# Performance work log

Measured on AMD Instinct MI355X. Metric: run time of the kernel, lower is better.

The kernel has to match this reference:

```python
import jax, jax.numpy as jnp
import numpy as np

DAMPENING = 50.0
THR = 1.0
TAU = 10.0
DECAY = float(np.exp(-1.0 / TAU))
V_MIN = -1.0


@jax.custom_vjp
def spike_fn(v_scaled):
    # Heaviside spike with surrogate (triangular) gradient
    return (v_scaled > 0.0).astype(v_scaled.dtype)

def _spike_fwd(v_scaled):
    return spike_fn(v_scaled), v_scaled

def _spike_bwd(v_scaled, dy):
    return (dy * DAMPENING * jnp.maximum(0.0, 1.0 - jnp.abs(v_scaled)),)

spike_fn.defvjp(_spike_fwd, _spike_bwd)


def setup_inputs() -> dict:
    key = jax.random.key(0)
    T, B, N_IN, N = 256, 32, 256, 2048
    ks = jax.random.split(key, 4)
    x = jax.random.normal(ks[0], (T, B, N_IN), jnp.float32)
    W_in = jax.random.normal(ks[1], (N_IN, N), jnp.float32) * (1.0 / np.sqrt(N_IN))
    b = jnp.zeros((N,), jnp.float32)
    # original uses stddev 1/sqrt(n_in) for Bernoulli_weights as well
    W_bern = jax.random.normal(ks[2], (N, N), jnp.float32) * (1.0 / np.sqrt(N_IN))
    random_indices = jax.random.randint(ks[3], (T, N), 0, N)
    return {"x": x, "W_in": W_in, "b": b, "W_bern": W_bern,
            "random_indices": random_indices}


def reference(x, W_in, b, W_bern, random_indices):
    # x: [T, B, n_in]; states v, z2: [B, n]
    B, N = x.shape[1], W_in.shape[1]
    v0 = jnp.zeros((B, N), x.dtype)
    z2_0 = jnp.zeros((B, N), x.dtype)  # old_spike state (unused in math, as in original)

    def step(carry, inp):
        v, _old_z2 = carry
        xt, idx = inp
        i_in = xt @ W_in + b                               # [B, n]
        new_v = jnp.clip(DECAY * v + i_in, V_MIN, THR + 0.01)
        z = spike_fn(new_v - THR)                          # spikes [B, n]
        new_v = jnp.where(z > 0.0, V_MIN, new_v)           # hard reset
        z2 = jnp.take(z @ W_bern, idx, axis=1)             # stochastic projection + column gather
        return (new_v, z2), (z, new_v, z2)

    _, (zs, vs, z2s) = jax.lax.scan(step, (v0, z2_0), (x, random_indices))
    return jnp.stack([zs, vs, z2s], axis=0)  # [3, T, B, n]
```

## Files before the change

### kernel.cpp

```cpp
#include <hip/hip_runtime.h>
#include <hip/hip_bf16.h>
#include <stdint.h>


#define T_STEPS 256
#define BATCH   32
#define NIN     256
#define NN      2048
#define BN_FLAT (BATCH * NN)
#define TBN     (T_STEPS * BATCH * NN)
#define MROWS   (T_STEPS * BATCH)

typedef __attribute__((ext_vector_type(4))) float fx4;
typedef __attribute__((ext_vector_type(4))) int   ix4;

__device__ __forceinline__ void gll16(const void* g, void* l) {
  typedef __attribute__((address_space(1))) void gvoid_t;
  typedef __attribute__((address_space(3))) void lvoid_t;
  __builtin_amdgcn_global_load_lds((gvoid_t*)(g), (lvoid_t*)(l), 16, 0, 0);
}

__device__ __forceinline__ void mfma16(fx4& d, ix4 a, ix4 b) {
  asm volatile("v_mfma_f32_16x16x32_bf16 %0, %1, %2, %0" : "+v"(d) : "v"(a), "v"(b));
}

__global__ __launch_bounds__(256) void xt_k(const float* __restrict__ X,
                                            float* __restrict__ Xt) {
  __shared__ float tile[32][33];
  const int m0 = blockIdx.x << 5, k0 = blockIdx.y << 5;
  const int tx = threadIdx.x, ty = threadIdx.y;
#pragma unroll
  for (int i = 0; i < 32; i += 8)
    tile[ty + i][tx] = X[(size_t)(m0 + ty + i) * NIN + k0 + tx];
  __syncthreads();
#pragma unroll
  for (int i = 0; i < 32; i += 8)
    Xt[(size_t)(k0 + ty + i) * MROWS + m0 + tx] = tile[tx][ty + i];
}

__global__ __launch_bounds__(256) void wt_convert(const float* __restrict__ W,
                                                  __hip_bfloat16* __restrict__ Wt) {
  __shared__ float tile[32][33];
  const int k0 = blockIdx.y << 5, n0 = blockIdx.x << 5;
  const int tx = threadIdx.x, ty = threadIdx.y;
#pragma unroll
  for (int i = 0; i < 32; i += 8)
    tile[ty + i][tx] = W[(size_t)(k0 + ty + i) * NN + n0 + tx];
  __syncthreads();
#pragma unroll
  for (int i = 0; i < 32; i += 8)
    Wt[(size_t)(n0 + ty + i) * NN + k0 + tx] = __float2bfloat16(tile[tx][ty + i]);
}

__global__ __launch_bounds__(256) void in_gemm(const float* __restrict__ Xt,
                                               const float* __restrict__ Wi,
                                               const float* __restrict__ bias,
                                               float* __restrict__ I) {
  __shared__ __align__(16) float As[16 * 64];
  __shared__ __align__(16) float Bs[16 * 128];
  const int tid = threadIdx.x;
  const int tm = tid >> 4;
  const int tn = tid & 15;
  const int m0 = blockIdx.x * 64, n0 = blockIdx.y * 128;

  fx4 acc[4][2] = {};

  const float* gA = Xt + (size_t)(tid >> 4) * MROWS + m0 + (tid & 15) * 4;
  const float* gB = Wi + (size_t)(tid >> 5) * NN + n0 + (tid & 31) * 4;
  char* lA = (char*)As + tid * 16;
  char* lB = (char*)Bs + tid * 16;

  for (int k0 = 0; k0 < NIN; k0 += 16) {
    gll16(gA, lA);
    gll16(gB, lB);
    gll16(gB + 8 * NN, lB + 4096);
    gA += (size_t)16 * MROWS;
    gB += (size_t)16 * NN;
    __syncthreads();
#pragma unroll
    for (int kk = 0; kk < 16; ++kk) {
      fx4 a  = *(const fx4*)&As[kk * 64 + tm * 4];
      fx4 b0 = *(const fx4*)&Bs[kk * 128 + tn * 4];
      fx4 b1 = *(const fx4*)&Bs[kk * 128 + 64 + tn * 4];
#pragma unroll
      for (int r = 0; r < 4; ++r)
#pragma unroll
        for (int c = 0; c < 4; ++c) {
          acc[r][0][c] = fmaf(a[r], b0[c], acc[r][0][c]);
          acc[r][1][c] = fmaf(a[r], b1[c], acc[r][1][c]);
        }
    }
    __syncthreads();
  }

#pragma unroll
  for (int r = 0; r < 4; ++r) {
    const size_t row = (size_t)(m0 + tm * 4 + r) * NN;
    fx4 r0, r1;
#pragma unroll
    for (int c = 0; c < 4; ++c) {
      r0[c] = acc[r][0][c] + bias[n0 + tn * 4 + c];
      r1[c] = acc[r][1][c] + bias[n0 + 64 + tn * 4 + c];
    }
    *(fx4*)&I[row + n0 + tn * 4] = r0;
    *(fx4*)&I[row + n0 + 64 + tn * 4] = r1;
  }
}

__device__ __forceinline__ void scan_body(float* zs, float* vsout,
                                          const float* I, __hip_bfloat16* Zb) {
  const int nid = blockIdx.x * 256 + threadIdx.x;
  float v = 0.f;
  for (int t0 = 0; t0 < T_STEPS; t0 += 8) {
    float iin[8];
#pragma unroll
    for (int u = 0; u < 8; ++u)
      iin[u] = I[(size_t)(t0 + u) * BN_FLAT + nid];
#pragma unroll
    for (int u = 0; u < 8; ++u) {
      float nv = __fadd_rn(__fmul_rn(0.9048374180359595f, v), iin[u]);
      nv = fminf(fmaxf(nv, -1.0f), 1.01f);
      const bool sp = nv > 1.0f;
      const float z = sp ? 1.0f : 0.0f;
      nv = sp ? -1.0f : nv;
      const size_t off = (size_t)(t0 + u) * BN_FLAT + nid;
      zs[off] = z;
      vsout[off] = nv;
      Zb[off] = __float2bfloat16(z);
      v = nv;
    }
  }
}

__global__ __launch_bounds__(256) void scan_sep(float* __restrict__ out,
                                                const float* __restrict__ I,
                                                __hip_bfloat16* __restrict__ Zb) {
  scan_body(out, out + (size_t)TBN, I, Zb);
}

__global__ __launch_bounds__(256) void scan_inp(float* out, __hip_bfloat16* Zb) {
  scan_body(out, out + (size_t)TBN, out + (size_t)TBN, Zb);
}

__global__ __launch_bounds__(256) void bern_gemm(const __hip_bfloat16* __restrict__ Z,
                                                 const __hip_bfloat16* __restrict__ Wt,
                                                 float* __restrict__ Y) {
  __shared__ __align__(16) __hip_bfloat16 Asm[128 * 32];
  __shared__ __align__(16) __hip_bfloat16 Bsm[128 * 32];
  const int tid = threadIdx.x;
  const int lane = tid & 63;
  const int wid = tid >> 6;
  const int wr = wid >> 1, wc = wid & 1;
  const int m0 = blockIdx.x * 128, n0 = blockIdx.y * 128;

  fx4 acc[4][4] = {};

  const int trow = tid >> 2;
  const int tcol = (tid & 3) << 4;
  const char* gA = (const char*)Z + ((size_t)(m0 + trow) << 12) + tcol;
  const char* gB = (const char*)Wt + ((size_t)(n0 + trow) << 12) + tcol;
  char* lA = (char*)Asm + tid * 16;
  char* lB = (char*)Bsm + tid * 16;

  const ix4* Au = (const ix4*)Asm;
  const ix4* Bu = (const ix4*)Bsm;
  const int abase = (wr * 64 + (lane & 15)) * 4 + (lane >> 4);
  const int bbase = (wc * 64 + (lane & 15)) * 4 + (lane >> 4);

  for (int ks = 0; ks < 64; ++ks) {
    gll16(gA, lA);
    gll16(gA + (size_t)64 * 4096, lA + 4096);
    gll16(gB, lB);
    gll16(gB + (size_t)64 * 4096, lB + 4096);
    gA += 64;
    gB += 64;
    __syncthreads();

    ix4 af[4], bf[4];
#pragma unroll
    for (int i = 0; i < 4; ++i) af[i] = Au[abase + i * 64];
#pragma unroll
    for (int i = 0; i < 4; ++i) bf[i] = Bu[bbase + i * 64];
#pragma unroll
    for (int mf = 0; mf < 4; ++mf)
#pragma unroll
      for (int nf = 0; nf < 4; ++nf)
        mfma16(acc[mf][nf], af[mf], bf[nf]);
    __syncthreads();
  }

  asm volatile("s_nop 7\n\ts_nop 7");

  const int crow = (lane >> 4) * 4;
  const int ccol = lane & 15;
#pragma unroll
  for (int mf = 0; mf < 4; ++mf)
#pragma unroll
    for (int nf = 0; nf < 4; ++nf)
#pragma unroll
      for (int j = 0; j < 4; ++j) {
        const int r = m0 + wr * 64 + mf * 16 + crow + j;
        const int c = n0 + wc * 64 + nf * 16 + ccol;
        Y[(size_t)r * NN + c] = acc[mf][nf][j];
      }
}

__global__ __launch_bounds__(256) void gather_k(float* __restrict__ Y,
                                                const int* __restrict__ ridx) {
  __shared__ __align__(16) float rowbuf[NN];
  const int tb = blockIdx.x;
  const int t = tb >> 5;
  float* yrow = Y + (size_t)tb * NN;
  const int tid = threadIdx.x;
#pragma unroll
  for (int i = 0; i < 2; ++i) {
    int u = tid + i * 256;
    ((fx4*)rowbuf)[u] = ((const fx4*)yrow)[u];
  }
  __syncthreads();
  const int* ir = ridx + t * NN;
#pragma unroll
  for (int i = 0; i < 8; ++i) {
    int j = tid + i * 256;
    yrow[j] = rowbuf[ir[j]];
  }
}

extern "C" void kernel_launch(void* const* d_in, const int* in_sizes, int n_in,
                              void* d_out, int out_size, void* d_ws, size_t ws_size,
                              hipStream_t stream) {
  const float* x      = (const float*)d_in[0];
  const float* W_in   = (const float*)d_in[1];
  const float* bias   = (const float*)d_in[2];
  const float* W_bern = (const float*)d_in[3];
  const int*   ridx   = (const int*)d_in[4];
  float* out = (float*)d_out;
  char* ws = (char*)d_ws;

  __hip_bfloat16* Wt = (__hip_bfloat16*)ws;
  __hip_bfloat16* Zb = (__hip_bfloat16*)(ws + (size_t)8388608);
  const size_t offI = 41943040;
  const bool sep = ws_size >= (size_t)109051904;
  float* Ibuf = sep ? (float*)(ws + offI) : (out + (size_t)TBN);

  float* Xt = out;

  xt_k<<<dim3(256, 8), dim3(32, 8), 0, stream>>>(x, Xt);
  wt_convert<<<dim3(64, 64), dim3(32, 8), 0, stream>>>(W_bern, Wt);
  in_gemm<<<dim3(128, 16), dim3(256), 0, stream>>>(Xt, W_in, bias, Ibuf);
  if (sep)
    scan_sep<<<dim3(256), dim3(256), 0, stream>>>(out, Ibuf, Zb);
  else
    scan_inp<<<dim3(256), dim3(256), 0, stream>>>(out, Zb);
  bern_gemm<<<dim3(64, 16), dim3(256), 0, stream>>>(Zb, Wt, out + (size_t)2 * TBN);
  gather_k<<<dim3(8192), dim3(256), 0, stream>>>(out + (size_t)2 * TBN, ridx);
}
```

Measured before the change: 253.0 us.

## Rewrite Bernoulli GEMM with 256x256 tiles, double-buffered LDS, and swizzled loads

```diff
diff --git a/kernel.cpp b/kernel.cpp
--- a/kernel.cpp
+++ b/kernel.cpp
@@ -142,66 +142,109 @@
   scan_body(out, out + (size_t)TBN, out + (size_t)TBN, Zb);
 }
 
-__global__ __launch_bounds__(256) void bern_gemm(const __hip_bfloat16* __restrict__ Z,
-                                                 const __hip_bfloat16* __restrict__ Wt,
-                                                 float* __restrict__ Y) {
-  __shared__ __align__(16) __hip_bfloat16 Asm[128 * 32];
-  __shared__ __align__(16) __hip_bfloat16 Bsm[128 * 32];
+__global__ __launch_bounds__(512, 2) void bern_gemm(const __hip_bfloat16* __restrict__ Z,
+                                                    const __hip_bfloat16* __restrict__ Wt,
+                                                    float* __restrict__ Y) {
+  __shared__ __align__(16) char lds[131072];
   const int tid = threadIdx.x;
-  const int lane = tid & 63;
-  const int wid = tid >> 6;
-  const int wr = wid >> 1, wc = wid & 1;
-  const int m0 = blockIdx.x * 128, n0 = blockIdx.y * 128;
-
-  fx4 acc[4][4] = {};
-
-  const int trow = tid >> 2;
-  const int tcol = (tid & 3) << 4;
-  const char* gA = (const char*)Z + ((size_t)(m0 + trow) << 12) + tcol;
-  const char* gB = (const char*)Wt + ((size_t)(n0 + trow) << 12) + tcol;
-  char* lA = (char*)Asm + tid * 16;
-  char* lB = (char*)Bsm + tid * 16;
-
-  const ix4* Au = (const ix4*)Asm;
-  const ix4* Bu = (const ix4*)Bsm;
-  const int abase = (wr * 64 + (lane & 15)) * 4 + (lane >> 4);
-  const int bbase = (wc * 64 + (lane & 15)) * 4 + (lane >> 4);
-
-  for (int ks = 0; ks < 64; ++ks) {
-    gll16(gA, lA);
-    gll16(gA + (size_t)64 * 4096, lA + 4096);
-    gll16(gB, lB);
-    gll16(gB + (size_t)64 * 4096, lB + 4096);
-    gA += 64;
-    gB += 64;
-    __syncthreads();
-
-    ix4 af[4], bf[4];
-#pragma unroll
-    for (int i = 0; i < 4; ++i) af[i] = Au[abase + i * 64];
-#pragma unroll
-    for (int i = 0; i < 4; ++i) bf[i] = Bu[bbase + i * 64];
-#pragma unroll
-    for (int mf = 0; mf < 4; ++mf)
-#pragma unroll
-      for (int nf = 0; nf < 4; ++nf)
-        mfma16(acc[mf][nf], af[mf], bf[nf]);
-    __syncthreads();
-  }
-
-  asm volatile("s_nop 7\n\ts_nop 7");
-
-  const int crow = (lane >> 4) * 4;
-  const int ccol = lane & 15;
-#pragma unroll
-  for (int mf = 0; mf < 4; ++mf)
-#pragma unroll
-    for (int nf = 0; nf < 4; ++nf)
+  const int l = tid & 63, wid = tid >> 6;
+  const int wr = wid >> 2, wc = wid & 3;
+  const int l15 = l & 15, l4 = l >> 4;
+  const int swz = (l & 7) << 4;
+  const int colp[2] = { (l4 * 16) ^ swz, (64 + l4 * 16) ^ swz };
+  const int m0 = blockIdx.x * 256, n0 = blockIdx.y * 256;
+  const int aoff = wr * 16384 + l15 * 128;
+  const int boff = 65536 + (wc >> 1) * 16384 + ((wc & 1) * 64 + l15) * 128;
+  const int colsel = ((tid & 7) ^ ((tid >> 3) & 7)) * 16;
+  const char* gA_ = (const char*)Z + ((size_t)(m0 + (tid >> 3)) << 12) + colsel;
+  const char* gB_ = (const char*)Wt + ((size_t)(n0 + (tid >> 3)) << 12) + colsel;
+
+  fx4 acc[8][4] = {};
+  ix4 af[4][2], bf[4][2];
+
+#define STAGE_A(tt, h)                                                       \
+  do {                                                                       \
+    const char* g = gA_ + ((size_t)((h) * 128) << 12) + (size_t)(tt) * 128;  \
+    char* d = lds + (((tt) & 1) * 32768) + (h) * 16384 + tid * 16;           \
+    gll16(g, d);                                                             \
+    gll16(g + ((size_t)64 << 12), d + 8192);                                 \
+  } while (0)
+#define STAGE_B(tt, h)                                                       \
+  do {                                                                       \
+    const char* g = gB_ + ((size_t)((h) * 128) << 12) + (size_t)(tt) * 128;  \
+    char* d = lds + 65536 + (((tt) & 1) * 32768) + (h) * 16384 + tid * 16;   \
+    gll16(g, d);                                                             \
+    gll16(g + ((size_t)64 << 12), d + 8192);                                 \
+  } while (0)
+#define LDA(mh)                                                              \
+  _Pragma("unroll") for (int mf = 0; mf < 4; ++mf)                           \
+    _Pragma("unroll") for (int ks = 0; ks < 2; ++ks)                         \
+      af[mf][ks] = *(const ix4*)(lb + aoff + ((mh)*4 + mf) * 2048 + colp[ks]);
+#define LDB(nh)                                                              \
+  _Pragma("unroll") for (int nf = 0; nf < 2; ++nf)                           \
+    _Pragma("unroll") for (int ks = 0; ks < 2; ++ks)                         \
+      bf[(nh)*2 + nf][ks] = *(const ix4*)(lb + boff + ((nh)*2 + nf) * 2048 + colp[ks]);
+#define MFMA_QUAD(mh, nh)                                                    \
+  do {                                                                       \
+    __builtin_amdgcn_s_setprio(1);                                           \
+    _Pragma("unroll") for (int ks = 0; ks < 2; ++ks)                         \
+      _Pragma("unroll") for (int mf = 0; mf < 4; ++mf)                       \
+        _Pragma("unroll") for (int nf = 0; nf < 2; ++nf)                     \
+          mfma16(acc[(mh)*4 + mf][(nh)*2 + nf], af[mf][ks], bf[(nh)*2 + nf][ks]); \
+    __builtin_amdgcn_s_setprio(0);                                           \
+  } while (0)
+#define SBAR asm volatile("s_barrier" ::: "memory")
+
+  STAGE_A(0, 0); STAGE_A(0, 1); STAGE_B(0, 0); STAGE_B(0, 1);
+  STAGE_B(1, 0); STAGE_B(1, 1);
+  asm volatile("s_waitcnt vmcnt(4)" ::: "memory");
+  SBAR;
+
+  for (int t = 0; t < 32; ++t) {
+    const char* lb = lds + (t & 1) * 32768;
+    LDA(0); LDB(0);
+    if (t < 31) STAGE_A(t + 1, 0);
+    SBAR;
+    asm volatile("s_waitcnt lgkmcnt(0)" ::: "memory");
+    MFMA_QUAD(0, 0);
+    SBAR;
+    LDB(1);
+    if (t < 31) STAGE_A(t + 1, 1);
+    SBAR;
+    asm volatile("s_waitcnt lgkmcnt(0)" ::: "memory");
+    MFMA_QUAD(0, 1);
+    SBAR;
+    LDA(1);
+    if (t < 30) STAGE_B(t + 2, 0);
+    SBAR;
+    asm volatile("s_waitcnt lgkmcnt(0)" ::: "memory");
+    MFMA_QUAD(1, 0);
+    SBAR;
+    if (t < 30) STAGE_B(t + 2, 1);
+    SBAR;
+    MFMA_QUAD(1, 1);
+    if (t < 30) asm volatile("s_waitcnt vmcnt(4)" ::: "memory");
+    else        asm volatile("s_waitcnt vmcnt(0)" ::: "memory");
+    SBAR;
+  }
+
+#undef STAGE_A
+#undef STAGE_B
+#undef LDA
+#undef LDB
+#undef MFMA_QUAD
+#undef SBAR
+
+  const int crow = l4 * 4;
+#pragma unroll
+  for (int MF = 0; MF < 8; ++MF)
+#pragma unroll
+    for (int NF = 0; NF < 4; ++NF)
 #pragma unroll
       for (int j = 0; j < 4; ++j) {
-        const int r = m0 + wr * 64 + mf * 16 + crow + j;
-        const int c = n0 + wc * 64 + nf * 16 + ccol;
-        Y[(size_t)r * NN + c] = acc[mf][nf][j];
+        const int r = m0 + wr * 128 + MF * 16 + crow + j;
+        const int c = n0 + wc * 64 + NF * 16 + l15;
+        Y[(size_t)r * NN + c] = acc[MF][NF][j];
       }
 }
 
@@ -252,6 +295,6 @@
     scan_sep<<<dim3(256), dim3(256), 0, stream>>>(out, Ibuf, Zb);
   else
     scan_inp<<<dim3(256), dim3(256), 0, stream>>>(out, Zb);
-  bern_gemm<<<dim3(64, 16), dim3(256), 0, stream>>>(Zb, Wt, out + (size_t)2 * TBN);
+  bern_gemm<<<dim3(32, 8), dim3(512), 0, stream>>>(Zb, Wt, out + (size_t)2 * TBN);
   gather_k<<<dim3(8192), dim3(256), 0, stream>>>(out + (size_t)2 * TBN, ridx);
 }
```

Result: faster. 238.4 us (-5.8%).
